# Kernel tuning notes

Measured on AMD Instinct MI355X. Metric: run time of the kernel, lower is better.

Reference implementation:

```python
import jax, jax.numpy as jnp
import numpy as np
import math

BS, SEQ, DIM, H, LK = 4, 4096, 768, 12, 256
HD = DIM // H  # 64
WIN = SEQ // LK  # 16, AdaptiveAvgPool1d reduces to uniform windows since SEQ % LK == 0


def setup_inputs() -> dict:
    key = jax.random.key(0)
    ks = jax.random.split(key, 12)
    s = 1.0 / math.sqrt(DIM)
    return {
        "query": jax.random.normal(ks[0], (BS, SEQ, DIM), jnp.float32),
        "key": jax.random.normal(ks[1], (BS, SEQ, DIM), jnp.float32),
        "value": jax.random.normal(ks[2], (BS, SEQ, DIM), jnp.float32),
        "mask": jax.random.normal(ks[3], (BS, SEQ), jnp.float32),  # mask<0 -> padded
        "Wq": jax.random.normal(ks[4], (DIM, DIM), jnp.float32) * s,
        "bq": jnp.zeros((DIM,), jnp.float32),
        "Wk": jax.random.normal(ks[5], (DIM, DIM), jnp.float32) * s,
        "bk": jnp.zeros((DIM,), jnp.float32),
        "Wv": jax.random.normal(ks[6], (DIM, DIM), jnp.float32) * s,
        "bv": jnp.zeros((DIM,), jnp.float32),
        "Wo": jax.random.normal(ks[7], (DIM, DIM), jnp.float32) * s,
        "bo": jnp.zeros((DIM,), jnp.float32),
    }


def reference(query, key, value, mask, Wq, bq, Wk, bk, Wv, bv, Wo, bo):
    bs, q_len, _ = query.shape
    # projections (nn.Linear: x @ W.T + b)
    Q = query @ Wq.T + bq
    K = key @ Wk.T + bk
    V = value @ Wv.T + bv
    # mask-fill padded K/V rows with 0 (mask dim==2 path: bool_mask = mask < 0)
    keep = (mask >= 0)[:, :, None]  # [bs, seq, 1]
    K = jnp.where(keep, K, 0.0)
    V = jnp.where(keep, V, 0.0)
    # adaptive avg pool over sequence -> linformer_k=256 (uniform windows of 16)
    Kc = K.reshape(bs, LK, WIN, DIM).mean(axis=2)  # [bs, 256, dim]
    Vc = V.reshape(bs, LK, WIN, DIM).mean(axis=2)
    # split heads
    Qh = Q.reshape(bs, q_len, H, HD) / math.sqrt(HD)  # scale fused
    Kh = Kc.reshape(bs, LK, H, HD)
    Vh = Vc.reshape(bs, LK, H, HD)
    # low-rank attention: [bs, h, q_len, 256]
    scores = jnp.einsum("bqhd,bkhd->bhqk", Qh, Kh)
    weights = jax.nn.softmax(scores, axis=-1)
    context = jnp.einsum("bhqk,bkhd->bqhd", weights, Vh).reshape(bs, q_len, DIM)
    return context @ Wo.T + bo
```

## Files before the change

### kernel.cpp

```cpp
#include <hip/hip_runtime.h>

#define BS_   4
#define SEQ_  4096
#define DIM_  768
#define NH_   12
#define HD_   64
#define LK_   256

typedef __attribute__((ext_vector_type(8))) short          bf8;
typedef __attribute__((ext_vector_type(8))) unsigned short us8;
typedef __attribute__((ext_vector_type(4))) unsigned short us4;
typedef __attribute__((ext_vector_type(4))) float          f32x4;

typedef unsigned int u32g __attribute__((address_space(1)));
typedef unsigned int u32l __attribute__((address_space(3)));

#define LOG2E 1.44269504088896340736f

__device__ __forceinline__ unsigned short f2bf(float f) {
  unsigned u = __builtin_bit_cast(unsigned, f);
  u += 0x7fffu + ((u >> 16) & 1u);
  return (unsigned short)(u >> 16);
}

__device__ __forceinline__ us8 cvt8(const float* __restrict__ p) {
  const float4 a = *(const float4*)p;
  const float4 b = *(const float4*)(p + 4);
  us8 r;
  r[0] = f2bf(a.x); r[1] = f2bf(a.y); r[2] = f2bf(a.z); r[3] = f2bf(a.w);
  r[4] = f2bf(b.x); r[5] = f2bf(b.y); r[6] = f2bf(b.z); r[7] = f2bf(b.w);
  return r;
}

__device__ __forceinline__ f32x4 max4(f32x4 a, f32x4 b) {
  f32x4 r;
  r[0] = fmaxf(a[0], b[0]); r[1] = fmaxf(a[1], b[1]);
  r[2] = fmaxf(a[2], b[2]); r[3] = fmaxf(a[3], b[3]);
  return r;
}

__global__ __launch_bounds__(256) void cvtbf_kernel(
    const float* __restrict__ Wq, const float* __restrict__ Wk,
    const float* __restrict__ Wv, const float* __restrict__ Wo,
    unsigned short* __restrict__ Wbf)
{
  const int i = blockIdx.x * 256 + threadIdx.x;
  const int WN8 = (DIM_ * DIM_) / 8;
  int j = i;
  const float* src; unsigned short* dst;
  if      (j <     WN8) { src = Wq; dst = Wbf;                   }
  else if (j < 2 * WN8) { src = Wk; dst = Wbf + DIM_*DIM_;     j -=     WN8; }
  else if (j < 3 * WN8) { src = Wv; dst = Wbf + 2*DIM_*DIM_;   j -= 2 * WN8; }
  else if (j < 4 * WN8) { src = Wo; dst = Wbf + 3*DIM_*DIM_;   j -= 3 * WN8; }
  else return;
  *(us8*)(dst + (size_t)j * 8) = cvt8(src + (size_t)j * 8);
}

__global__ __launch_bounds__(384) void pool_kernel(
    const float* __restrict__ key, const float* __restrict__ value,
    const float* __restrict__ mask,
    unsigned short* __restrict__ pk, unsigned short* __restrict__ pv,
    float* __restrict__ frac)
{
  const int blk = blockIdx.x;
  const int b = blk >> 8;
  const int l = blk & 255;
  const int tid = threadIdx.x;
  __shared__ float keep[16];
  if (tid < 16) keep[tid] = (mask[b * SEQ_ + l * 16 + tid] >= 0.f) ? 1.f : 0.f;
  __syncthreads();
  const int isV = tid >= 192;
  const int c = isV ? tid - 192 : tid;
  const float* src = isV ? value : key;
  float4 acc = make_float4(0.f, 0.f, 0.f, 0.f);
  #pragma unroll 1
  for (int w = 0; w < 16; ++w) {
    if (keep[w] != 0.f) {
      const float4 v = *(const float4*)(src + (size_t)(b * SEQ_ + l * 16 + w) * DIM_ + c * 4);
      acc.x += v.x; acc.y += v.y; acc.z += v.z; acc.w += v.w;
    }
  }
  const float s = 1.f / 16.f;
  unsigned short* dst = isV ? pv : pk;
  us4 o4;
  o4[0] = f2bf(acc.x * s); o4[1] = f2bf(acc.y * s);
  o4[2] = f2bf(acc.z * s); o4[3] = f2bf(acc.w * s);
  *(us4*)(dst + (size_t)(b * LK_ + l) * DIM_ + c * 4) = o4;
  if (tid == 0) {
    float cnt = 0.f;
    for (int w = 0; w < 16; ++w) cnt += keep[w];
    frac[b * LK_ + l] = cnt * s;
  }
}

template<int SA, int MODE, int SWZ>
__global__ __launch_bounds__(256) void gemm_bt(
    const void* __restrict__ Aptr_, const void* __restrict__ Bptr_,
    const float* __restrict__ bias, const float* __restrict__ bias2,
    const float* __restrict__ frac,
    void* __restrict__ Cout, float scale)
{
  constexpr int K = DIM_;
  __shared__ __align__(16) unsigned short lA[128 * 32];
  __shared__ __align__(16) unsigned short lB[128 * 32];
  const int tid  = threadIdx.x;
  const int lane = tid & 63;
  const int wave = tid >> 6;

  int bx, by;
  if (SWZ) {
    const int r = (blockIdx.x & 7) * 96 + (blockIdx.x >> 3);
    bx = r / 6; by = r % 6;
  } else {
    bx = blockIdx.x; by = blockIdx.y;
  }
  const int brow = bx * 128;
  const int bcol = by * 128;

  const unsigned short* A = (const unsigned short*)Aptr_;
  const float*          Af = (const float*)Aptr_;
  const unsigned short* Bw = (const unsigned short*)Bptr_;
  const float* bb = bias;
  int isV = 0;
  if (MODE == 34) {
    isV = blockIdx.z;
    A  += (size_t)isV * (BS_ * LK_ * DIM_);
    Bw += (size_t)isV * (DIM_ * DIM_);
    if (isV) bb = bias2;
  }

  const int wr   = (wave >> 1) * 64;
  const int wc   = (wave & 1) * 64;
  const int fr   = lane & 15;
  const int fk   = (lane >> 4) * 8;

  f32x4 acc[4][4];
  #pragma unroll
  for (int i = 0; i < 4; ++i)
    #pragma unroll
    for (int j = 0; j < 4; ++j) acc[i][j] = (f32x4){0.f, 0.f, 0.f, 0.f};

  const int srow = tid >> 2;
  const int schk = (tid & 3) * 8;

  for (int k0 = 0; k0 < K; k0 += 32) {
    us8 a0, a1;
    if (SA == 1) {
      a0 = cvt8(Af + (size_t)(brow + srow) * K + k0 + schk);
      a1 = cvt8(Af + (size_t)(brow + srow + 64) * K + k0 + schk);
    }
    __syncthreads();
    if (SA == 0) {
      __builtin_amdgcn_global_load_lds(
          (const u32g*)(A + (size_t)(brow + srow) * K + k0 + schk),
          (u32l*)&lA[tid * 8], 16, 0, 0);
      __builtin_amdgcn_global_load_lds(
          (const u32g*)(A + (size_t)(brow + srow + 64) * K + k0 + schk),
          (u32l*)&lA[2048 + tid * 8], 16, 0, 0);
    } else {
      *(us8*)&lA[tid * 8]        = a0;
      *(us8*)&lA[2048 + tid * 8] = a1;
    }
    __builtin_amdgcn_global_load_lds(
        (const u32g*)(Bw + (size_t)(bcol + srow) * K + k0 + schk),
        (u32l*)&lB[tid * 8], 16, 0, 0);
    __builtin_amdgcn_global_load_lds(
        (const u32g*)(Bw + (size_t)(bcol + srow + 64) * K + k0 + schk),
        (u32l*)&lB[2048 + tid * 8], 16, 0, 0);
    __syncthreads();
    bf8 af[4], bfv[4];
    #pragma unroll
    for (int mi = 0; mi < 4; ++mi)
      af[mi] = *(const bf8*)&lA[(wr + mi * 16 + fr) * 32 + fk];
    #pragma unroll
    for (int ni = 0; ni < 4; ++ni)
      bfv[ni] = *(const bf8*)&lB[(wc + ni * 16 + fr) * 32 + fk];
    #pragma unroll
    for (int mi = 0; mi < 4; ++mi)
      #pragma unroll
      for (int ni = 0; ni < 4; ++ni)
        acc[mi][ni] = __builtin_amdgcn_mfma_f32_16x16x32_bf16(af[mi], bfv[ni], acc[mi][ni], 0, 0, 0);
  }

  const int er = (lane >> 4) * 4;
  #pragma unroll
  for (int mi = 0; mi < 4; ++mi) {
    #pragma unroll
    for (int ni = 0; ni < 4; ++ni) {
      #pragma unroll
      for (int j = 0; j < 4; ++j) {
        const int r = brow + wr + mi * 16 + er + j;
        const int c = bcol + wc + ni * 16 + fr;
        float v = acc[mi][ni][j];
        if (MODE == 0) {
          v = (v + bias[c]) * scale;
          ((unsigned short*)Cout)[(size_t)r * DIM_ + c] = f2bf(v);
        } else if (MODE == 2) {
          ((float*)Cout)[(size_t)r * DIM_ + c] = v + bias[c];
        } else {
          v += frac[r] * bb[c];
          const int bb_ = r >> 8, key = r & 255;
          const int hh = c >> 6, dd = c & 63;
          const int bh = bb_ * NH_ + hh;
          size_t idx;
          if (isV) {
            idx = (size_t)bh * 16384 +
                ((key >> 5) * 4 + (dd >> 4)) * 512 + ((key >> 3) & 3) * 128 +
                (dd & 15) * 8 + (key & 7) + 786432;
          } else {
            const int t = key >> 5, g = (key >> 3) & 3, sub = (key >> 2) & 1, jj = key & 3;
            const int frk = g * 4 + jj;
            idx = (size_t)bh * 16384 +
                (((t * 2 + sub) * 2) + (dd >> 5)) * 512 + ((dd >> 3) & 3) * 128 +
                frk * 8 + (dd & 7);
          }
          ((unsigned short*)Cout)[idx] = f2bf(v);
        }
      }
    }
  }
}

__global__ __launch_bounds__(1024, 4) void attn_fused(
    const unsigned short* __restrict__ Qh,
    const unsigned short* __restrict__ Kf,
    const unsigned short* __restrict__ Vf,
    unsigned short* __restrict__ ctx)
{
  __shared__ __align__(16) unsigned short Ks[16384];
  __shared__ __align__(16) unsigned short Vs[16384];
  const int tid  = threadIdx.x;
  const int lane = tid & 63;
  const int wave = tid >> 6;
  const int bh = blockIdx.y;
  const int b = bh / NH_, h = bh % NH_;
  const int fr = lane & 15;
  const int hi = lane >> 4;
  const int qrow = blockIdx.x * 256 + wave * 16;

  {
    const unsigned short* kg = Kf + (size_t)bh * 16384 + tid * 8;
    const unsigned short* vg = Vf + (size_t)bh * 16384 + tid * 8;
    __builtin_amdgcn_global_load_lds((const u32g*)kg,          (u32l*)&Ks[tid * 8],        16, 0, 0);
    __builtin_amdgcn_global_load_lds((const u32g*)(kg + 8192), (u32l*)&Ks[8192 + tid * 8], 16, 0, 0);
    __builtin_amdgcn_global_load_lds((const u32g*)vg,          (u32l*)&Vs[tid * 8],        16, 0, 0);
    __builtin_amdgcn_global_load_lds((const u32g*)(vg + 8192), (u32l*)&Vs[8192 + tid * 8], 16, 0, 0);
  }

  const unsigned short* qp = Qh + (size_t)(b * SEQ_ + qrow + fr) * DIM_ + h * HD_ + hi * 8;
  const bf8 q0 = *(const bf8*)qp;
  const bf8 q1 = *(const bf8*)(qp + 32);

  __syncthreads();

  f32x4 scA[8], scB[8];
  __builtin_amdgcn_s_setprio(1);
  #pragma unroll
  for (int s = 0; s < 8; ++s) {
    const bf8 ka0 = *(const bf8*)&Ks[(s * 4 + 0) * 512 + lane * 8];
    const bf8 ka1 = *(const bf8*)&Ks[(s * 4 + 1) * 512 + lane * 8];
    const bf8 kb0 = *(const bf8*)&Ks[(s * 4 + 2) * 512 + lane * 8];
    const bf8 kb1 = *(const bf8*)&Ks[(s * 4 + 3) * 512 + lane * 8];
    f32x4 x = (f32x4){0.f, 0.f, 0.f, 0.f};
    x = __builtin_amdgcn_mfma_f32_16x16x32_bf16(ka0, q0, x, 0, 0, 0);
    x = __builtin_amdgcn_mfma_f32_16x16x32_bf16(ka1, q1, x, 0, 0, 0);
    scA[s] = x;
    f32x4 y = (f32x4){0.f, 0.f, 0.f, 0.f};
    y = __builtin_amdgcn_mfma_f32_16x16x32_bf16(kb0, q0, y, 0, 0, 0);
    y = __builtin_amdgcn_mfma_f32_16x16x32_bf16(kb1, q1, y, 0, 0, 0);
    scB[s] = y;
  }
  __builtin_amdgcn_s_setprio(0);

  f32x4 tm[8];
  #pragma unroll
  for (int s = 0; s < 8; ++s) tm[s] = max4(scA[s], scB[s]);
  tm[0] = max4(tm[0], tm[4]); tm[1] = max4(tm[1], tm[5]);
  tm[2] = max4(tm[2], tm[6]); tm[3] = max4(tm[3], tm[7]);
  tm[0] = max4(tm[0], tm[2]); tm[1] = max4(tm[1], tm[3]);
  tm[0] = max4(tm[0], tm[1]);
  float m = fmaxf(fmaxf(tm[0][0], tm[0][1]), fmaxf(tm[0][2], tm[0][3]));
  m = fmaxf(m, __shfl_xor(m, 16));
  m = fmaxf(m, __shfl_xor(m, 32));

  f32x4 uA = (f32x4){0.f, 0.f, 0.f, 0.f};
  f32x4 uB = (f32x4){0.f, 0.f, 0.f, 0.f};
  #pragma unroll
  for (int s = 0; s < 8; ++s) {
    #pragma unroll
    for (int j = 0; j < 4; ++j) {
      scA[s][j] = exp2f(scA[s][j] - m);
      scB[s][j] = exp2f(scB[s][j] - m);
    }
    uA += scA[s];
    uB += scB[s];
  }
  const f32x4 uv = uA + uB;
  float sum = (uv[0] + uv[1]) + (uv[2] + uv[3]);
  sum += __shfl_xor(sum, 16);
  sum += __shfl_xor(sum, 32);
  const float inv = 1.f / sum;

  bf8 pa[8];
  #pragma unroll
  for (int s = 0; s < 8; ++s) {
    bf8 p;
    #pragma unroll
    for (int j = 0; j < 4; ++j) {
      p[j]     = (short)f2bf(scA[s][j] * inv);
      p[4 + j] = (short)f2bf(scB[s][j] * inv);
    }
    pa[s] = p;
  }

  f32x4 acc[4];
  #pragma unroll
  for (int ct = 0; ct < 4; ++ct) acc[ct] = (f32x4){0.f, 0.f, 0.f, 0.f};
  __builtin_amdgcn_s_setprio(1);
  #pragma unroll
  for (int s = 0; s < 8; ++s) {
    #pragma unroll
    for (int ct = 0; ct < 4; ++ct) {
      const bf8 vf = *(const bf8*)&Vs[(s * 4 + ct) * 512 + lane * 8];
      acc[ct] = __builtin_amdgcn_mfma_f32_16x16x32_bf16(pa[s], vf, acc[ct], 0, 0, 0);
    }
  }
  __builtin_amdgcn_s_setprio(0);

  #pragma unroll
  for (int ct = 0; ct < 4; ++ct)
    #pragma unroll
    for (int j = 0; j < 4; ++j)
      ctx[(size_t)(b * SEQ_ + qrow + hi * 4 + j) * DIM_ + h * HD_ + ct * 16 + fr] =
          f2bf(acc[ct][j]);
}

extern "C" void kernel_launch(void* const* d_in, const int* in_sizes, int n_in,
                              void* d_out, int out_size, void* d_ws, size_t ws_size,
                              hipStream_t stream) {
  const float* query = (const float*)d_in[0];
  const float* key   = (const float*)d_in[1];
  const float* value = (const float*)d_in[2];
  const float* mask  = (const float*)d_in[3];
  const float* Wq    = (const float*)d_in[4];
  const float* bq    = (const float*)d_in[5];
  const float* Wk    = (const float*)d_in[6];
  const float* bk    = (const float*)d_in[7];
  const float* Wv    = (const float*)d_in[8];
  const float* bv    = (const float*)d_in[9];
  const float* Wo    = (const float*)d_in[10];
  const float* bo    = (const float*)d_in[11];
  float* out = (float*)d_out;

  char* ws = (char*)d_ws;
  unsigned short* Qh  = (unsigned short*)ws;
  unsigned short* ctx = (unsigned short*)(ws + 25165824);
  unsigned short* pK  = (unsigned short*)(ws + 50331648);
  unsigned short* pV  = (unsigned short*)(ws + 51904512);
  unsigned short* Kf  = (unsigned short*)(ws + 53477376);
  unsigned short* Vf  = (unsigned short*)(ws + 55050240);
  float*          frac = (float*)(ws + 56623104);
  unsigned short* Wbf = (unsigned short*)(ws + 56627200);

  const float qscale = 0.125f * LOG2E;

  pool_kernel<<<dim3(1024), dim3(384), 0, stream>>>(key, value, mask, pK, pV, frac);
  cvtbf_kernel<<<dim3(1152), dim3(256), 0, stream>>>(Wq, Wk, Wv, Wo, Wbf);
  gemm_bt<1, 0, 1><<<dim3(768), dim3(256), 0, stream>>>(
      query, Wbf, bq, nullptr, nullptr, Qh, qscale);
  gemm_bt<0, 34, 0><<<dim3(8, 6, 2), dim3(256), 0, stream>>>(
      pK, Wbf + DIM_*DIM_, bk, bv, frac, Kf, 1.f);
  attn_fused<<<dim3(16, 48), dim3(1024), 0, stream>>>(Qh, Kf, Vf, ctx);
  gemm_bt<0, 2, 1><<<dim3(768), dim3(256), 0, stream>>>(
      ctx, Wbf + 3*DIM_*DIM_, bo, nullptr, nullptr, out, 1.f);
}
```

Measured before the change: 137.6 us.

## Double-buffer GEMM LDS tiles and XOR-swizzle K chunks to avoid bank conflicts

The bf16 GEMM main loop now uses two LDS buffers, so the global-to-LDS load of the next K tile is issued before the MFMAs on the current tile. This drops one of the two barriers per iteration and hides load latency. The 8-element K chunks are also XOR-swizzled by row, on both the store and the fragment read, to reduce LDS bank conflicts. LDS use doubles, which may lower occupancy. Correctness depends on the swizzle matching between writer and reader and on the single barrier per iteration being enough.

```diff
diff --git a/kernel.cpp b/kernel.cpp
--- a/kernel.cpp
+++ b/kernel.cpp
@@ -101,8 +101,9 @@
     void* __restrict__ Cout, float scale)
 {
   constexpr int K = DIM_;
-  __shared__ __align__(16) unsigned short lA[128 * 32];
-  __shared__ __align__(16) unsigned short lB[128 * 32];
+  constexpr int NT = K / 32;
+  __shared__ __align__(16) unsigned short lA[2][4096];
+  __shared__ __align__(16) unsigned short lB[2][4096];
   const int tid  = threadIdx.x;
   const int lane = tid & 63;
   const int wave = tid >> 6;
@@ -132,7 +133,8 @@
   const int wr   = (wave >> 1) * 64;
   const int wc   = (wave & 1) * 64;
   const int fr   = lane & 15;
-  const int fk   = (lane >> 4) * 8;
+  const int rg   = (fr >> 1) & 3;
+  const int cph  = ((lane >> 4) ^ rg) * 8;
 
   f32x4 acc[4][4];
   #pragma unroll
@@ -141,46 +143,68 @@
     for (int j = 0; j < 4; ++j) acc[i][j] = (f32x4){0.f, 0.f, 0.f, 0.f};
 
   const int srow = tid >> 2;
-  const int schk = (tid & 3) * 8;
-
-  for (int k0 = 0; k0 < K; k0 += 32) {
-    us8 a0, a1;
-    if (SA == 1) {
-      a0 = cvt8(Af + (size_t)(brow + srow) * K + k0 + schk);
-      a1 = cvt8(Af + (size_t)(brow + srow + 64) * K + k0 + schk);
-    }
-    __syncthreads();
+  const int schk = (((tid & 3) ^ ((srow >> 1) & 3))) * 8;
+
+  auto STAGE = [&](int k0, int b) {
     if (SA == 0) {
       __builtin_amdgcn_global_load_lds(
           (const u32g*)(A + (size_t)(brow + srow) * K + k0 + schk),
-          (u32l*)&lA[tid * 8], 16, 0, 0);
+          (u32l*)&lA[b][tid * 8], 16, 0, 0);
       __builtin_amdgcn_global_load_lds(
           (const u32g*)(A + (size_t)(brow + srow + 64) * K + k0 + schk),
-          (u32l*)&lA[2048 + tid * 8], 16, 0, 0);
-    } else {
-      *(us8*)&lA[tid * 8]        = a0;
-      *(us8*)&lA[2048 + tid * 8] = a1;
+          (u32l*)&lA[b][2048 + tid * 8], 16, 0, 0);
     }
     __builtin_amdgcn_global_load_lds(
         (const u32g*)(Bw + (size_t)(bcol + srow) * K + k0 + schk),
-        (u32l*)&lB[tid * 8], 16, 0, 0);
+        (u32l*)&lB[b][tid * 8], 16, 0, 0);
     __builtin_amdgcn_global_load_lds(
         (const u32g*)(Bw + (size_t)(bcol + srow + 64) * K + k0 + schk),
-        (u32l*)&lB[2048 + tid * 8], 16, 0, 0);
-    __syncthreads();
+        (u32l*)&lB[b][2048 + tid * 8], 16, 0, 0);
+  };
+
+  auto COMPUTE = [&](int b) {
     bf8 af[4], bfv[4];
     #pragma unroll
     for (int mi = 0; mi < 4; ++mi)
-      af[mi] = *(const bf8*)&lA[(wr + mi * 16 + fr) * 32 + fk];
+      af[mi] = *(const bf8*)&lA[b][(wr + mi * 16 + fr) * 32 + cph];
     #pragma unroll
     for (int ni = 0; ni < 4; ++ni)
-      bfv[ni] = *(const bf8*)&lB[(wc + ni * 16 + fr) * 32 + fk];
+      bfv[ni] = *(const bf8*)&lB[b][(wc + ni * 16 + fr) * 32 + cph];
     #pragma unroll
     for (int mi = 0; mi < 4; ++mi)
       #pragma unroll
       for (int ni = 0; ni < 4; ++ni)
         acc[mi][ni] = __builtin_amdgcn_mfma_f32_16x16x32_bf16(af[mi], bfv[ni], acc[mi][ni], 0, 0, 0);
-  }
+  };
+
+  if (SA == 1) {
+    const us8 a0 = cvt8(Af + (size_t)(brow + srow) * K + schk);
+    const us8 a1 = cvt8(Af + (size_t)(brow + srow + 64) * K + schk);
+    *(us8*)&lA[0][tid * 8]        = a0;
+    *(us8*)&lA[0][2048 + tid * 8] = a1;
+  }
+  STAGE(0, 0);
+  __syncthreads();
+
+  int buf = 0;
+  #pragma unroll 2
+  for (int t = 0; t < NT - 1; ++t) {
+    const int k1 = (t + 1) * 32;
+    us8 a0, a1;
+    if (SA == 1) {
+      a0 = cvt8(Af + (size_t)(brow + srow) * K + k1 + schk);
+      a1 = cvt8(Af + (size_t)(brow + srow + 64) * K + k1 + schk);
+    }
+    STAGE(k1, buf ^ 1);
+    COMPUTE(buf);
+    if (SA == 1) {
+      *(us8*)&lA[buf ^ 1][tid * 8]        = a0;
+      *(us8*)&lA[buf ^ 1][2048 + tid * 8] = a1;
+    }
+    __syncthreads();
+    buf ^= 1;
+  }
+  COMPUTE(buf);
 
   const int er = (lane >> 4) * 4;
   #pragma unroll
```

New measurement: 137.3 us. About the same (-0.2%).

## Pre-convert query to bf16 and widen GEMM K-tile with XOR-swizzled LDS

Applied to the files above, without the earlier changes.

The query tensor is now converted to bf16 in the existing conversion kernel, written into the ctx buffer, which is free at that point. That lets the Q projection GEMM use the same direct global-to-LDS loads as the other GEMMs instead of converting fp32 in registers. The GEMM K-tile grows from 32 to 64, halving the number of barrier pairs per block, and an XOR swizzle on LDS chunk placement is meant to avoid bank conflicts on fragment reads. The cost is an extra pass that writes and rereads a 24 MB bf16 copy of query, and twice the LDS per block.

```diff
diff --git a/kernel.cpp b/kernel.cpp
--- a/kernel.cpp
+++ b/kernel.cpp
@@ -40,13 +40,16 @@
 }
 
 __global__ __launch_bounds__(256) void cvtbf_kernel(
+    const float* __restrict__ query,
     const float* __restrict__ Wq, const float* __restrict__ Wk,
     const float* __restrict__ Wv, const float* __restrict__ Wo,
-    unsigned short* __restrict__ Wbf)
+    unsigned short* __restrict__ Qbf, unsigned short* __restrict__ Wbf)
 {
   const int i = blockIdx.x * 256 + threadIdx.x;
+  const int QN8 = (BS_ * SEQ_ * DIM_) / 8;
   const int WN8 = (DIM_ * DIM_) / 8;
-  int j = i;
+  if (i < QN8) { *(us8*)(Qbf + (size_t)i * 8) = cvt8(query + (size_t)i * 8); return; }
+  int j = i - QN8;
   const float* src; unsigned short* dst;
   if      (j <     WN8) { src = Wq; dst = Wbf;                   }
   else if (j < 2 * WN8) { src = Wk; dst = Wbf + DIM_*DIM_;     j -=     WN8; }
@@ -93,16 +96,18 @@
   }
 }
 
-template<int SA, int MODE, int SWZ>
+template<int MODE, int SWZ>
 __global__ __launch_bounds__(256) void gemm_bt(
     const void* __restrict__ Aptr_, const void* __restrict__ Bptr_,
     const float* __restrict__ bias, const float* __restrict__ bias2,
     const float* __restrict__ frac,
     void* __restrict__ Cout, float scale)
 {
-  constexpr int K = DIM_;
-  __shared__ __align__(16) unsigned short lA[128 * 32];
-  __shared__ __align__(16) unsigned short lB[128 * 32];
+  constexpr int K  = DIM_;
+  constexpr int BK = 64;
+  constexpr int NT = K / BK;
+  __shared__ __align__(16) unsigned short lA[128 * BK];
+  __shared__ __align__(16) unsigned short lB[128 * BK];
   const int tid  = threadIdx.x;
   const int lane = tid & 63;
   const int wave = tid >> 6;
@@ -117,8 +122,7 @@
   const int brow = bx * 128;
   const int bcol = by * 128;
 
-  const unsigned short* A = (const unsigned short*)Aptr_;
-  const float*          Af = (const float*)Aptr_;
+  const unsigned short* A  = (const unsigned short*)Aptr_;
   const unsigned short* Bw = (const unsigned short*)Bptr_;
   const float* bb = bias;
   int isV = 0;
@@ -129,10 +133,11 @@
     if (isV) bb = bias2;
   }
 
-  const int wr   = (wave >> 1) * 64;
-  const int wc   = (wave & 1) * 64;
-  const int fr   = lane & 15;
-  const int fk   = (lane >> 4) * 8;
+  const int wr = (wave >> 1) * 64;
+  const int wc = (wave & 1) * 64;
+  const int fr = lane & 15;
+  const int hi = lane >> 4;
+  const int rx = fr & 7;
 
   f32x4 acc[4][4];
   #pragma unroll
@@ -140,46 +145,39 @@
     #pragma unroll
     for (int j = 0; j < 4; ++j) acc[i][j] = (f32x4){0.f, 0.f, 0.f, 0.f};
 
-  const int srow = tid >> 2;
-  const int schk = (tid & 3) * 8;
-
-  for (int k0 = 0; k0 < K; k0 += 32) {
-    us8 a0, a1;
-    if (SA == 1) {
-      a0 = cvt8(Af + (size_t)(brow + srow) * K + k0 + schk);
-      a1 = cvt8(Af + (size_t)(brow + srow + 64) * K + k0 + schk);
-    }
+  const int srow = tid >> 3;
+  const int schk = ((tid & 7) ^ (srow & 7)) * 8;
+
+  for (int t = 0; t < NT; ++t) {
+    const int k0 = t * BK;
     __syncthreads();
-    if (SA == 0) {
+    #pragma unroll
+    for (int s = 0; s < 4; ++s) {
       __builtin_amdgcn_global_load_lds(
-          (const u32g*)(A + (size_t)(brow + srow) * K + k0 + schk),
-          (u32l*)&lA[tid * 8], 16, 0, 0);
+          (const u32g*)(A + (size_t)(brow + srow + s * 32) * K + k0 + schk),
+          (u32l*)&lA[s * 2048 + tid * 8], 16, 0, 0);
       __builtin_amdgcn_global_load_lds(
-          (const u32g*)(A + (size_t)(brow + srow + 64) * K + k0 + schk),
-          (u32l*)&lA[2048 + tid * 8], 16, 0, 0);
-    } else {
-      *(us8*)&lA[tid * 8]        = a0;
-      *(us8*)&lA[2048 + tid * 8] = a1;
-    }
-    __builtin_amdgcn_global_load_lds(
-        (const u32g*)(Bw + (size_t)(bcol + srow) * K + k0 + schk),
-        (u32l*)&lB[tid * 8], 16, 0, 0);
-    __builtin_amdgcn_global_load_lds(
-        (const u32g*)(Bw + (size_t)(bcol + srow + 64) * K + k0 + schk),
-        (u32l*)&lB[2048 + tid * 8], 16, 0, 0);
+          (const u32g*)(Bw + (size_t)(bcol + srow + s * 32) * K + k0 + schk),
+          (u32l*)&lB[s * 2048 + tid * 8], 16, 0, 0);
+    }
     __syncthreads();
-    bf8 af[4], bfv[4];
-    #pragma unroll
-    for (int mi = 0; mi < 4; ++mi)
-      af[mi] = *(const bf8*)&lA[(wr + mi * 16 + fr) * 32 + fk];
-    #pragma unroll
-    for (int ni = 0; ni < 4; ++ni)
-      bfv[ni] = *(const bf8*)&lB[(wc + ni * 16 + fr) * 32 + fk];
-    #pragma unroll
-    for (int mi = 0; mi < 4; ++mi)
+    #pragma unroll
+    for (int ks = 0; ks < 2; ++ks) {
+      bf8 af[4], bfv[4];
+      const int c = ks * 4 + hi;
+      const int pc = (c ^ rx) * 8;
+      #pragma unroll
+      for (int mi = 0; mi < 4; ++mi)
+        af[mi] = *(const bf8*)&lA[(wr + mi * 16 + fr) * BK + pc];
       #pragma unroll
       for (int ni = 0; ni < 4; ++ni)
-        acc[mi][ni] = __builtin_amdgcn_mfma_f32_16x16x32_bf16(af[mi], bfv[ni], acc[mi][ni], 0, 0, 0);
+        bfv[ni] = *(const bf8*)&lB[(wc + ni * 16 + fr) * BK + pc];
+      #pragma unroll
+      for (int mi = 0; mi < 4; ++mi)
+        #pragma unroll
+        for (int ni = 0; ni < 4; ++ni)
+          acc[mi][ni] = __builtin_amdgcn_mfma_f32_16x16x32_bf16(af[mi], bfv[ni], acc[mi][ni], 0, 0, 0);
+    }
   }
 
   const int er = (lane >> 4) * 4;
@@ -208,10 +206,10 @@
                 ((key >> 5) * 4 + (dd >> 4)) * 512 + ((key >> 3) & 3) * 128 +
                 (dd & 15) * 8 + (key & 7) + 786432;
           } else {
-            const int t = key >> 5, g = (key >> 3) & 3, sub = (key >> 2) & 1, jj = key & 3;
+            const int tt = key >> 5, g = (key >> 3) & 3, sub = (key >> 2) & 1, jj = key & 3;
             const int frk = g * 4 + jj;
             idx = (size_t)bh * 16384 +
-                (((t * 2 + sub) * 2) + (dd >> 5)) * 512 + ((dd >> 3) & 3) * 128 +
+                (((tt * 2 + sub) * 2) + (dd >> 5)) * 512 + ((dd >> 3) & 3) * 128 +
                 frk * 8 + (dd & 7);
           }
           ((unsigned short*)Cout)[idx] = f2bf(v);
@@ -361,16 +359,17 @@
   unsigned short* Vf  = (unsigned short*)(ws + 55050240);
   float*          frac = (float*)(ws + 56623104);
   unsigned short* Wbf = (unsigned short*)(ws + 56627200);
+  unsigned short* Qbf = ctx;
 
   const float qscale = 0.125f * LOG2E;
 
   pool_kernel<<<dim3(1024), dim3(384), 0, stream>>>(key, value, mask, pK, pV, frac);
-  cvtbf_kernel<<<dim3(1152), dim3(256), 0, stream>>>(Wq, Wk, Wv, Wo, Wbf);
-  gemm_bt<1, 0, 1><<<dim3(768), dim3(256), 0, stream>>>(
-      query, Wbf, bq, nullptr, nullptr, Qh, qscale);
-  gemm_bt<0, 34, 0><<<dim3(8, 6, 2), dim3(256), 0, stream>>>(
+  cvtbf_kernel<<<dim3(7296), dim3(256), 0, stream>>>(query, Wq, Wk, Wv, Wo, Qbf, Wbf);
+  gemm_bt<0, 1><<<dim3(768), dim3(256), 0, stream>>>(
+      Qbf, Wbf, bq, nullptr, nullptr, Qh, qscale);
+  gemm_bt<34, 0><<<dim3(8, 6, 2), dim3(256), 0, stream>>>(
       pK, Wbf + DIM_*DIM_, bk, bv, frac, Kf, 1.f);
   attn_fused<<<dim3(16, 48), dim3(1024), 0, stream>>>(Qh, Kf, Vf, ctx);
-  gemm_bt<0, 2, 1><<<dim3(768), dim3(256), 0, stream>>>(
+  gemm_bt<2, 1><<<dim3(768), dim3(256), 0, stream>>>(
       ctx, Wbf + 3*DIM_*DIM_, bo, nullptr, nullptr, out, 1.f);
 }
```

New measurement: 140.5 us. 1.02x slower.
